# Optimization experiments

Hardware: AMD Instinct MI355X
Metric: run time of the kernel (lower is better)

## Reference

```python
import jax, jax.numpy as jnp
import numpy as np

HEADS = 12
HEAD_DIM = 64
WINDOW = 65  # must be odd
EMBED = 768
B, L = 1, 2048


def setup_inputs() -> dict:
    key = jax.random.key(0)
    k1, k2, k3 = jax.random.split(key, 3)
    x = jax.random.normal(k1, (B, L, EMBED), dtype=jnp.float32)
    w_qkv = jax.random.normal(k2, (EMBED, 3 * HEADS * HEAD_DIM), dtype=jnp.float32) * 0.02
    w_out = jax.random.normal(k3, (HEADS * HEAD_DIM, EMBED), dtype=jnp.float32) * 0.02
    b_out = jnp.zeros((EMBED,), dtype=jnp.float32)
    return {"x": x, "w_qkv": w_qkv, "w_out": w_out, "b_out": b_out}


def reference(x, w_qkv, w_out, b_out):
    b, l, _ = x.shape
    pad = WINDOW // 2
    # qkv projection (no bias), reshape to [B, L, H, 3*Dh], split as in TF code
    qkv = jnp.einsum('ble,ef->blf', x, w_qkv).reshape(b, l, HEADS, 3 * HEAD_DIM)
    q = qkv[..., :HEAD_DIM]                      # [B, L, H, Dh]
    k = qkv[..., HEAD_DIM:2 * HEAD_DIM]
    v = qkv[..., 2 * HEAD_DIM:]
    # zero-pad along sequence (matches tf.pad; padded positions participate in softmax)
    k_pad = jnp.pad(k, ((0, 0), (pad, pad), (0, 0), (0, 0)))  # [B, L+2p, H, Dh]
    v_pad = jnp.pad(v, ((0, 0), (pad, pad), (0, 0), (0, 0)))
    # sliding windows via a single gather: [B, L, W, H, Dh]
    idx = jnp.arange(l)[:, None] + jnp.arange(WINDOW)[None, :]
    k_win = k_pad[:, idx]
    v_win = v_pad[:, idx]
    score = jnp.einsum('blhd,blwhd->blhw', q, k_win) / jnp.sqrt(
        jnp.asarray(HEAD_DIM, dtype=x.dtype))
    weights = jax.nn.softmax(score, axis=-1)      # [B, L, H, W]
    out = jnp.einsum('blhw,blwhd->blhd', weights, v_win)
    out = out.reshape(b, l, HEADS * HEAD_DIM)
    return jnp.einsum('blf,fe->ble', out, w_out) + b_out
```

## Files before the change

### kernel.cpp

```cpp
#include <hip/hip_runtime.h>
#include <hip/hip_bf16.h>

#define HEADS 12
#define HD 64
#define PADW 32
#define EMBED 768
#define LSEQ 2048
#define QKV_N (3 * HEADS * HD)
#define LPAD (LSEQ + 64)

typedef short short8 __attribute__((ext_vector_type(8)));
typedef short short4v __attribute__((ext_vector_type(4)));
typedef float f32x4 __attribute__((ext_vector_type(4)));

__device__ short g_xb[LSEQ * EMBED];
__device__ short g_wqkvT[QKV_N * EMBED];
__device__ short g_woutT[EMBED * EMBED];
__device__ short g_qkvb[LSEQ * QKV_N];
__device__ short g_vT[HEADS * HD * LPAD];
__device__ short g_attnb[LSEQ * EMBED];

__device__ __forceinline__ short f2bf(float f) {
  unsigned x = __builtin_bit_cast(unsigned, f);
  x += 0x7fffu + ((x >> 16) & 1u);
  return (short)(x >> 16);
}

#define GLB(p) ((const __attribute__((address_space(1))) void*)(p))
#define LDS(p) ((__attribute__((address_space(3))) void*)(p))

#define PREP_A 1536
#define PREP_B 1728
#define PREP_C 576
#define PREP_D 24
#define PREP_TOT (PREP_A + PREP_B + PREP_C + PREP_D)

__global__ __launch_bounds__(256) void prep(
    const float* __restrict__ x, const float* __restrict__ w_qkv,
    const float* __restrict__ w_out, short* __restrict__ xb,
    short* __restrict__ wqkvT, short* __restrict__ woutT,
    short* __restrict__ vT) {
  __shared__ float T[32][33];
  const int b = blockIdx.x, tid = threadIdx.x;
  if (b < PREP_A) {
    int i = b * 256 + tid;
    float4 v = ((const float4*)x)[i];
    short4v o;
    o[0] = f2bf(v.x); o[1] = f2bf(v.y); o[2] = f2bf(v.z); o[3] = f2bf(v.w);
    ((short4v*)xb)[i] = o;
  } else if (b < PREP_A + PREP_B + PREP_C) {
    const float* W; short* WT; int N, bx, by;
    if (b < PREP_A + PREP_B) {
      int t = b - PREP_A; W = w_qkv; WT = wqkvT; N = QKV_N; bx = t % 72; by = t / 72;
    } else {
      int t = b - PREP_A - PREP_B; W = w_out; WT = woutT; N = EMBED; bx = t % 24; by = t / 24;
    }
    const int K = EMBED;
    int tx = tid & 31, ty = tid >> 5;
    int n0 = bx * 32, k0 = by * 32;
#pragma unroll
    for (int p = 0; p < 4; ++p)
      T[ty + p * 8][tx] = W[(size_t)(k0 + ty + p * 8) * N + n0 + tx];
    __syncthreads();
#pragma unroll
    for (int p = 0; p < 4; ++p)
      WT[(size_t)(n0 + ty + p * 8) * K + k0 + tx] = f2bf(T[tx][ty + p * 8]);
  } else {
    int j = (b - PREP_A - PREP_B - PREP_C) * 256 + tid;
    int hd = j >> 3, side = (j >> 2) & 1, off = (j & 3) * 8;
    short8 z = {};
    *(short8*)&vT[(size_t)hd * LPAD + side * 2080 + off] = z;
  }
}

template <bool OUT_BF16, bool FUSE_VT>
__global__ __launch_bounds__(256) void gemm_wp64(
    const short* __restrict__ A, const short* __restrict__ Bt,
    const float* __restrict__ bias, void* __restrict__ Cv,
    short* __restrict__ vT, int M, int N, int K) {
  __shared__ __align__(16) short lds_s[4 * 2 * 4096];

  const int tid = threadIdx.x;
  const int wv = tid >> 6, lane = tid & 63;
  const int wm = wv >> 1, wn = wv & 1;
  const int lanelo = lane & 15, quad = lane >> 4;
  const int m0 = blockIdx.y * 64 + wm * 32;
  const int n0 = blockIdx.x * 64 + wn * 32;
  const int srow8 = lane >> 3, schk = lane & 7;
  const int sgc = schk ^ srow8;
  const int xk = lanelo & 7;
  short* wlds = lds_s + wv * 2 * 4096;

  f32x4 acc[2][2] = {};

  auto stage = [&](int j, int buf) {
    short* Ab = wlds + buf * 4096;
    short* Bb = Ab + 2048;
    const int k0 = j * 64;
#pragma unroll
    for (int c = 0; c < 4; ++c) {
      int row = c * 8 + srow8;
      const short* ga = A + (size_t)(m0 + row) * K + k0 + sgc * 8;
      __builtin_amdgcn_global_load_lds(GLB(ga), LDS(&Ab[c * 8 * 64]), 16, 0, 0);
    }
#pragma unroll
    for (int c = 0; c < 4; ++c) {
      int row = c * 8 + srow8;
      const short* gb = Bt + (size_t)(n0 + row) * K + k0 + sgc * 8;
      __builtin_amdgcn_global_load_lds(GLB(gb), LDS(&Bb[c * 8 * 64]), 16, 0, 0);
    }
  };

  const int steps = K / 64;
  stage(0, 0);
  stage(1, 1);
  for (int j = 0; j < steps; ++j) {
    const int buf = j & 1;
    if (j < steps - 1) asm volatile("s_waitcnt vmcnt(8)" ::: "memory");
    else               asm volatile("s_waitcnt vmcnt(0)" ::: "memory");
    short* Ab = wlds + buf * 4096;
    short* Bb = Ab + 2048;
    short8 af[2][2], bfr[2][2];
#pragma unroll
    for (int ks = 0; ks < 2; ++ks) {
      int p = (ks * 4 + quad) ^ xk;
#pragma unroll
      for (int mt = 0; mt < 2; ++mt)
        af[ks][mt] = *(const short8*)&Ab[(mt * 16 + lanelo) * 64 + p * 8];
#pragma unroll
      for (int nt = 0; nt < 2; ++nt)
        bfr[ks][nt] = *(const short8*)&Bb[(nt * 16 + lanelo) * 64 + p * 8];
    }
    asm volatile("s_waitcnt lgkmcnt(0)" ::: "memory");
    if (j + 2 < steps) stage(j + 2, buf);
#pragma unroll
    for (int ks = 0; ks < 2; ++ks)
#pragma unroll
      for (int mt = 0; mt < 2; ++mt)
#pragma unroll
        for (int nt = 0; nt < 2; ++nt)
          acc[mt][nt] = __builtin_amdgcn_mfma_f32_16x16x32_bf16(
              af[ks][mt], bfr[ks][nt], acc[mt][nt], 0, 0, 0);
  }

  if (FUSE_VT) {
#pragma unroll
    for (int nt = 0; nt < 2; ++nt) {
      int c0 = n0 + nt * 16;
      if ((c0 % 192) >= 128) {
        int h = c0 / 192, d0 = (c0 % 192) - 128;
#pragma unroll
        for (int mt = 0; mt < 2; ++mt) {
          int d = d0 + lanelo;
          int row0 = m0 + mt * 16 + quad * 4;
          short4v o;
#pragma unroll
          for (int r = 0; r < 4; ++r) o[r] = f2bf(acc[mt][nt][r]);
          *(short4v*)&vT[(size_t)(h * 64 + d) * LPAD + PADW + row0] = o;
        }
      }
    }
  }

  if (OUT_BF16) {
    constexpr int ST = 40;
    short* eb = wlds;
#pragma unroll
    for (int mt = 0; mt < 2; ++mt)
#pragma unroll
      for (int nt = 0; nt < 2; ++nt) {
        int rloc = mt * 16 + quad * 4;
        int cloc = nt * 16 + lanelo;
#pragma unroll
        for (int r = 0; r < 4; ++r)
          eb[(rloc + r) * ST + cloc] = f2bf(acc[mt][nt][r]);
      }
    asm volatile("s_waitcnt lgkmcnt(0)" ::: "memory");
    short* Cc = (short*)Cv;
#pragma unroll
    for (int pass = 0; pass < 2; ++pass) {
      int u = pass * 64 + lane;
      int row = u >> 2, seg = u & 3;
      short8 vv = *(const short8*)&eb[row * ST + seg * 8];
      *(short8*)&Cc[(size_t)(m0 + row) * N + n0 + seg * 8] = vv;
    }
  } else {
    constexpr int ST = 36;
    float* fl = (float*)wlds;
#pragma unroll
    for (int mt = 0; mt < 2; ++mt)
#pragma unroll
      for (int nt = 0; nt < 2; ++nt) {
        int rloc = mt * 16 + quad * 4;
        int cloc = nt * 16 + lanelo;
#pragma unroll
        for (int r = 0; r < 4; ++r)
          fl[(rloc + r) * ST + cloc] = acc[mt][nt][r];
      }
    asm volatile("s_waitcnt lgkmcnt(0)" ::: "memory");
    float* Cc = (float*)Cv;
#pragma unroll
    for (int pass = 0; pass < 4; ++pass) {
      int u = pass * 64 + lane;
      int row = u >> 3, seg = u & 7;
      float4 vv = *(const float4*)&fl[row * ST + seg * 4];
      float4 bb = *(const float4*)&bias[n0 + seg * 4];
      vv.x += bb.x; vv.y += bb.y; vv.z += bb.z; vv.w += bb.w;
      *(float4*)&Cc[(size_t)(m0 + row) * N + n0 + seg * 4] = vv;
    }
  }
}

__global__ __launch_bounds__(256) void attn_mfma(
    const short* __restrict__ qkvb, const short* __restrict__ vT,
    short* __restrict__ attnb) {
  const int blk = blockIdx.x;
  const int h = blk % HEADS;
  const int l0 = (blk / HEADS) * 64;
  const int sb = l0 - PADW;

  const int tid = threadIdx.x;
  const int wv = tid >> 6, lane = tid & 63;
  const int lanelo = lane & 15, quad = lane >> 4;
  const int qoff = h * 192, koff = h * 192 + 64;

  __shared__ __align__(16) short P_lds[64 * 136];

  const short* qp = qkvb + (size_t)(l0 + wv * 16 + lanelo) * QKV_N + qoff;
  short8 aq0 = *(const short8*)(qp + quad * 8);
  short8 aq1 = *(const short8*)(qp + 32 + quad * 8);

  f32x4 sacc[8] = {};
#pragma unroll
  for (int nt = 0; nt < 8; ++nt) {
    int gl = sb + nt * 16 + lanelo;
    short8 bk0 = {}, bk1 = {};
    if ((unsigned)gl < (unsigned)LSEQ) {
      const short* kp = qkvb + (size_t)gl * QKV_N + koff;
      bk0 = *(const short8*)(kp + quad * 8);
      bk1 = *(const short8*)(kp + 32 + quad * 8);
    }
    sacc[nt] = __builtin_amdgcn_mfma_f32_16x16x32_bf16(aq0, bk0, sacc[nt], 0, 0, 0);
    sacc[nt] = __builtin_amdgcn_mfma_f32_16x16x32_bf16(aq1, bk1, sacc[nt], 0, 0, 0);
  }

  short8 bv[4][4];
#pragma unroll
  for (int ks = 0; ks < 4; ++ks) {
    int lp = l0 + ks * 32 + quad * 8;
#pragma unroll
    for (int nt = 0; nt < 4; ++nt) {
      int d = nt * 16 + lanelo;
      bv[ks][nt] = *(const short8*)&vT[((size_t)h * 64 + d) * LPAD + lp];
    }
  }

  float rsum[4] = {0.f, 0.f, 0.f, 0.f};
#pragma unroll
  for (int nt = 0; nt < 8; ++nt)
#pragma unroll
    for (int r = 0; r < 4; ++r) {
      int li = wv * 16 + quad * 4 + r;
      int widx = nt * 16 + lanelo - li;
      float s = (widx >= 0 && widx <= 64) ? sacc[nt][r] * 0.125f : -1e30f;
      float p = __expf(s);
      sacc[nt][r] = p;
      rsum[r] += p;
    }
#pragma unroll
  for (int r = 0; r < 4; ++r) {
#pragma unroll
    for (int off = 1; off < 16; off <<= 1)
      rsum[r] += __shfl_xor(rsum[r], off);
    rsum[r] = 1.f / rsum[r];
  }
#pragma unroll
  for (int nt = 0; nt < 8; ++nt)
#pragma unroll
    for (int r = 0; r < 4; ++r) {
      int row = wv * 16 + quad * 4 + r;
      P_lds[row * 136 + nt * 16 + lanelo] = f2bf(sacc[nt][r] * rsum[r]);
    }
  __syncthreads();

  f32x4 oacc[4] = {};
#pragma unroll
  for (int ks = 0; ks < 4; ++ks) {
    short8 ap = *(const short8*)&P_lds[(wv * 16 + lanelo) * 136 + ks * 32 + quad * 8];
#pragma unroll
    for (int nt = 0; nt < 4; ++nt)
      oacc[nt] = __builtin_amdgcn_mfma_f32_16x16x32_bf16(ap, bv[ks][nt], oacc[nt], 0, 0, 0);
  }

  __syncthreads();
#pragma unroll
  for (int nt = 0; nt < 4; ++nt)
#pragma unroll
    for (int r = 0; r < 4; ++r) {
      int row = wv * 16 + quad * 4 + r;
      P_lds[row * 80 + nt * 16 + lanelo] = f2bf(oacc[nt][r]);
    }
  __syncthreads();
#pragma unroll
  for (int rp = 0; rp < 64; rp += 32) {
    int row = rp + tid / 8, seg = tid % 8;
    short8 vv = *(const short8*)&P_lds[row * 80 + seg * 8];
    *(short8*)&attnb[(size_t)(l0 + row) * EMBED + h * 64 + seg * 8] = vv;
  }
}

extern "C" void kernel_launch(void* const* d_in, const int* in_sizes, int n_in,
                              void* d_out, int out_size, void* d_ws, size_t ws_size,
                              hipStream_t stream) {
  const float* x     = (const float*)d_in[0];
  const float* w_qkv = (const float*)d_in[1];
  const float* w_out = (const float*)d_in[2];
  const float* b_out = (const float*)d_in[3];
  float* out = (float*)d_out;

  short *xb, *wqkvT, *woutT, *qkvb, *vT, *attnb;
  (void)hipGetSymbolAddress((void**)&xb,    HIP_SYMBOL(g_xb));
  (void)hipGetSymbolAddress((void**)&wqkvT, HIP_SYMBOL(g_wqkvT));
  (void)hipGetSymbolAddress((void**)&woutT, HIP_SYMBOL(g_woutT));
  (void)hipGetSymbolAddress((void**)&qkvb,  HIP_SYMBOL(g_qkvb));
  (void)hipGetSymbolAddress((void**)&vT,    HIP_SYMBOL(g_vT));
  (void)hipGetSymbolAddress((void**)&attnb, HIP_SYMBOL(g_attnb));

  prep<<<PREP_TOT, 256, 0, stream>>>(x, w_qkv, w_out, xb, wqkvT, woutT, vT);

  gemm_wp64<true, true><<<dim3(QKV_N / 64, LSEQ / 64), 256, 0, stream>>>(
      xb, wqkvT, nullptr, qkvb, vT, LSEQ, QKV_N, EMBED);

  attn_mfma<<<(LSEQ / 64) * HEADS, 256, 0, stream>>>(qkvb, vT, attnb);

  gemm_wp64<false, false><<<dim3(EMBED / 64, LSEQ / 64), 256, 0, stream>>>(
      attnb, woutT, b_out, out, nullptr, LSEQ, EMBED, EMBED);
}
```

Measured before the change: 110.7 us.

## Load GEMM MFMA fragments directly from global into registers with triple buffering

Replaces the per-wave LDS staging (global_load_lds into swizzled LDS, then ds_read fragments) with direct global-to-register loads of the MFMA operand fragments, using a three-deep rotating register pipeline fully unrolled for K=768. LDS is shrunk to what the epilogue needs, which may raise occupancy and removes LDS round trips. The trade-off is that global loads are now 16-byte per-lane strided row accesses, which may coalesce less well, and register pressure rises.

```diff
diff --git a/kernel.cpp b/kernel.cpp
--- a/kernel.cpp
+++ b/kernel.cpp
@@ -25,9 +25,6 @@
   x += 0x7fffu + ((x >> 16) & 1u);
   return (short)(x >> 16);
 }
-
-#define GLB(p) ((const __attribute__((address_space(1))) void*)(p))
-#define LDS(p) ((__attribute__((address_space(3))) void*)(p))
 
 #define PREP_A 1536
 #define PREP_B 1728
@@ -73,12 +70,18 @@
   }
 }
 
+struct Frag {
+  short8 a00, a01, a10, a11;
+  short8 b00, b01, b10, b11;
+};
+
 template <bool OUT_BF16, bool FUSE_VT>
-__global__ __launch_bounds__(256) void gemm_wp64(
+__global__ __launch_bounds__(256) void gemm_reg64(
     const short* __restrict__ A, const short* __restrict__ Bt,
     const float* __restrict__ bias, void* __restrict__ Cv,
     short* __restrict__ vT, int M, int N, int K) {
-  __shared__ __align__(16) short lds_s[4 * 2 * 4096];
+  constexpr int WEPI = OUT_BF16 ? 32 * 40 : 32 * 36 * 2;
+  __shared__ __align__(16) short lds_s[4 * WEPI];
 
   const int tid = threadIdx.x;
   const int wv = tid >> 6, lane = tid & 63;
@@ -86,62 +89,51 @@
   const int lanelo = lane & 15, quad = lane >> 4;
   const int m0 = blockIdx.y * 64 + wm * 32;
   const int n0 = blockIdx.x * 64 + wn * 32;
-  const int srow8 = lane >> 3, schk = lane & 7;
-  const int sgc = schk ^ srow8;
-  const int xk = lanelo & 7;
-  short* wlds = lds_s + wv * 2 * 4096;
+  short* wlds = lds_s + wv * WEPI;
+
+  const short* pa0 = A + (size_t)(m0 + lanelo) * K + quad * 8;
+  const short* pa1 = A + (size_t)(m0 + 16 + lanelo) * K + quad * 8;
+  const short* pb0 = Bt + (size_t)(n0 + lanelo) * K + quad * 8;
+  const short* pb1 = Bt + (size_t)(n0 + 16 + lanelo) * K + quad * 8;
 
   f32x4 acc[2][2] = {};
 
-  auto stage = [&](int j, int buf) {
-    short* Ab = wlds + buf * 4096;
-    short* Bb = Ab + 2048;
-    const int k0 = j * 64;
-#pragma unroll
-    for (int c = 0; c < 4; ++c) {
-      int row = c * 8 + srow8;
-      const short* ga = A + (size_t)(m0 + row) * K + k0 + sgc * 8;
-      __builtin_amdgcn_global_load_lds(GLB(ga), LDS(&Ab[c * 8 * 64]), 16, 0, 0);
-    }
-#pragma unroll
-    for (int c = 0; c < 4; ++c) {
-      int row = c * 8 + srow8;
-      const short* gb = Bt + (size_t)(n0 + row) * K + k0 + sgc * 8;
-      __builtin_amdgcn_global_load_lds(GLB(gb), LDS(&Bb[c * 8 * 64]), 16, 0, 0);
-    }
+  auto loadstep = [&](Frag& f, int j) {
+    const int o = j * 64;
+    f.a00 = *(const short8*)(pa0 + o);
+    f.a01 = *(const short8*)(pa1 + o);
+    f.b00 = *(const short8*)(pb0 + o);
+    f.b01 = *(const short8*)(pb1 + o);
+    f.a10 = *(const short8*)(pa0 + o + 32);
+    f.a11 = *(const short8*)(pa1 + o + 32);
+    f.b10 = *(const short8*)(pb0 + o + 32);
+    f.b11 = *(const short8*)(pb1 + o + 32);
   };
-
-  const int steps = K / 64;
-  stage(0, 0);
-  stage(1, 1);
-  for (int j = 0; j < steps; ++j) {
-    const int buf = j & 1;
-    if (j < steps - 1) asm volatile("s_waitcnt vmcnt(8)" ::: "memory");
-    else               asm volatile("s_waitcnt vmcnt(0)" ::: "memory");
-    short* Ab = wlds + buf * 4096;
-    short* Bb = Ab + 2048;
-    short8 af[2][2], bfr[2][2];
-#pragma unroll
-    for (int ks = 0; ks < 2; ++ks) {
-      int p = (ks * 4 + quad) ^ xk;
-#pragma unroll
-      for (int mt = 0; mt < 2; ++mt)
-        af[ks][mt] = *(const short8*)&Ab[(mt * 16 + lanelo) * 64 + p * 8];
-#pragma unroll
-      for (int nt = 0; nt < 2; ++nt)
-        bfr[ks][nt] = *(const short8*)&Bb[(nt * 16 + lanelo) * 64 + p * 8];
-    }
-    asm volatile("s_waitcnt lgkmcnt(0)" ::: "memory");
-    if (j + 2 < steps) stage(j + 2, buf);
-#pragma unroll
-    for (int ks = 0; ks < 2; ++ks)
-#pragma unroll
-      for (int mt = 0; mt < 2; ++mt)
-#pragma unroll
-        for (int nt = 0; nt < 2; ++nt)
-          acc[mt][nt] = __builtin_amdgcn_mfma_f32_16x16x32_bf16(
-              af[ks][mt], bfr[ks][nt], acc[mt][nt], 0, 0, 0);
-  }
+  auto compute = [&](const Frag& f) {
+    acc[0][0] = __builtin_amdgcn_mfma_f32_16x16x32_bf16(f.a00, f.b00, acc[0][0], 0, 0, 0);
+    acc[0][1] = __builtin_amdgcn_mfma_f32_16x16x32_bf16(f.a00, f.b01, acc[0][1], 0, 0, 0);
+    acc[1][0] = __builtin_amdgcn_mfma_f32_16x16x32_bf16(f.a01, f.b00, acc[1][0], 0, 0, 0);
+    acc[1][1] = __builtin_amdgcn_mfma_f32_16x16x32_bf16(f.a01, f.b01, acc[1][1], 0, 0, 0);
+    acc[0][0] = __builtin_amdgcn_mfma_f32_16x16x32_bf16(f.a10, f.b10, acc[0][0], 0, 0, 0);
+    acc[0][1] = __builtin_amdgcn_mfma_f32_16x16x32_bf16(f.a10, f.b11, acc[0][1], 0, 0, 0);
+    acc[1][0] = __builtin_amdgcn_mfma_f32_16x16x32_bf16(f.a11, f.b10, acc[1][0], 0, 0, 0);
+    acc[1][1] = __builtin_amdgcn_mfma_f32_16x16x32_bf16(f.a11, f.b11, acc[1][1], 0, 0, 0);
+  };
+
+  Frag f0, f1, f2;
+  loadstep(f0, 0);
+  loadstep(f1, 1);
+#pragma unroll
+  for (int jj = 0; jj < 3; ++jj) {
+    const int j3 = jj * 3;
+    loadstep(f2, j3 + 2); compute(f0);
+    loadstep(f0, j3 + 3); compute(f1);
+    loadstep(f1, j3 + 4); compute(f2);
+  }
+  loadstep(f2, 11);
+  compute(f0);
+  compute(f1);
+  compute(f2);
 
   if (FUSE_VT) {
 #pragma unroll
@@ -328,11 +320,11 @@
 
   prep<<<PREP_TOT, 256, 0, stream>>>(x, w_qkv, w_out, xb, wqkvT, woutT, vT);
 
-  gemm_wp64<true, true><<<dim3(QKV_N / 64, LSEQ / 64), 256, 0, stream>>>(
+  gemm_reg64<true, true><<<dim3(QKV_N / 64, LSEQ / 64), 256, 0, stream>>>(
       xb, wqkvT, nullptr, qkvb, vT, LSEQ, QKV_N, EMBED);
 
   attn_mfma<<<(LSEQ / 64) * HEADS, 256, 0, stream>>>(qkvb, vT, attnb);
 
-  gemm_wp64<false, false><<<dim3(EMBED / 64, LSEQ / 64), 256, 0, stream>>>(
+  gemm_reg64<false, false><<<dim3(EMBED / 64, LSEQ / 64), 256, 0, stream>>>(
       attnb, woutT, b_out, out, nullptr, LSEQ, EMBED, EMBED);
 }
```

New measurement: 157.1 us. 41.9% more time.
